# Kernel tuning notes

Measured on AMD Instinct MI355X. Metric: run time of the kernel, lower is better.

The kernel has to match this reference:

```python
import jax, jax.numpy as jnp
import numpy as np

N = 100000
E = 1600000
IN_DIM = 20
HID = 32
HEADS = 4
OUT = 64
NEG_SLOPE = 0.2


def _p(key, shape, scale=0.1):
    return jax.random.normal(key, shape, dtype=jnp.float32) * scale


def setup_inputs() -> dict:
    key = jax.random.key(0)
    ks = jax.random.split(key, 20)
    x = jax.random.normal(ks[0], (N, IN_DIM), dtype=jnp.float32)
    edge_index = jax.random.randint(ks[1], (2, E), 0, N, dtype=jnp.int32)
    edge_attr = jax.random.uniform(ks[2], (E, 1), dtype=jnp.float32)
    HC1 = HEADS * HID
    return {
        "x": x,
        "edge_index": edge_index,
        "edge_attr": edge_attr,
        "Wl1": _p(ks[3], (HC1, IN_DIM)), "bl1": jnp.zeros((HC1,), jnp.float32),
        "Wr1": _p(ks[4], (HC1, IN_DIM)), "br1": jnp.zeros((HC1,), jnp.float32),
        "We1": _p(ks[5], (HC1, 1)),
        "att1": _p(ks[6], (HEADS, HID)),
        "b1": jnp.zeros((HC1,), jnp.float32),
        "Wl2": _p(ks[7], (OUT, HC1)), "bl2": jnp.zeros((OUT,), jnp.float32),
        "Wr2": _p(ks[8], (OUT, HC1)), "br2": jnp.zeros((OUT,), jnp.float32),
        "We2": _p(ks[9], (OUT, 1)),
        "att2": _p(ks[10], (1, OUT)),
        "b2": jnp.zeros((OUT,), jnp.float32),
    }


def gatv2_conv(x, src, dst, edge_attr, Wl, bl, Wr, br, We, att, bias, heads, ch, concat):
    n = x.shape[0]
    # add self loops; edge_attr fill_value = mean (PyG default)
    loop = jnp.arange(n, dtype=src.dtype)
    src = jnp.concatenate([src, loop])
    dst = jnp.concatenate([dst, loop])
    ea_fill = jnp.broadcast_to(edge_attr.mean(axis=0, keepdims=True), (n, edge_attr.shape[1]))
    edge_attr = jnp.concatenate([edge_attr, ea_fill], axis=0)

    xl = (x @ Wl.T + bl).reshape(n, heads, ch)   # source transform [N,H,C]
    xr = (x @ Wr.T + br).reshape(n, heads, ch)   # target transform [N,H,C]
    ee = (edge_attr @ We.T).reshape(-1, heads, ch)  # edge embed [E',H,C]

    e = xl[src] + xr[dst] + ee                    # [E',H,C]
    e = jax.nn.leaky_relu(e, NEG_SLOPE)
    logits = jnp.einsum('ehc,hc->eh', e, att)     # [E',H]

    # segment softmax over destination nodes (every node has a self loop)
    mx = jax.ops.segment_max(logits, dst, num_segments=n)
    ex = jnp.exp(logits - mx[dst])
    denom = jax.ops.segment_sum(ex, dst, num_segments=n)
    alpha = ex / denom[dst]                       # [E',H]

    msg = xl[src] * alpha[:, :, None]             # [E',H,C]
    out = jax.ops.segment_sum(msg, dst, num_segments=n)  # [N,H,C]
    out = out.reshape(n, heads * ch) if concat else out.mean(axis=1)
    return out + bias


def reference(x, edge_index, edge_attr, Wl1, bl1, Wr1, br1, We1, att1, b1,
              Wl2, bl2, Wr2, br2, We2, att2, b2):
    src, dst = edge_index[0], edge_index[1]
    h = gatv2_conv(x, src, dst, edge_attr, Wl1, bl1, Wr1, br1, We1, att1, b1,
                   HEADS, HID, concat=True)
    h = jax.nn.elu(h)  # dropout is identity in eval mode
    out = gatv2_conv(h, src, dst, edge_attr, Wl2, bl2, Wr2, br2, We2, att2, b2,
                     1, OUT, concat=False)
    return out
```

## Files before the change

### kernel.cpp

```cpp
#include <hip/hip_runtime.h>
#include <cstdint>
#include <cstddef>

#define NNODES 100000
#define NEDGES 1600000
#define IN_DIM 20
#define HID    32
#define HEADS  4
#define HC1    128
#define OUTC   64
#define NEG    0.2f
#define NCHUNK ((NNODES + 255) / 256)
#define NBLK   ((NNODES + 63) / 64)

__device__ __forceinline__ float lrelu(float v) { return v >= 0.0f ? v : NEG * v; }

typedef _Float16 h2 __attribute__((ext_vector_type(2)));
union U4H { uint4 u; h2 h[4]; };
union U2H { uint2 u; h2 h[2]; };

__global__ void k_sum(const float* __restrict__ ea, int n, float* __restrict__ out) {
    float s = 0.0f;
    for (int i = blockIdx.x * blockDim.x + threadIdx.x; i < n; i += gridDim.x * blockDim.x)
        s += ea[i];
    #pragma unroll
    for (int off = 32; off > 0; off >>= 1) s += __shfl_down(s, off, 64);
    __shared__ float ls[4];
    int lane = threadIdx.x & 63, wid = threadIdx.x >> 6;
    if (lane == 0) ls[wid] = s;
    __syncthreads();
    if (threadIdx.x == 0) {
        float t = ls[0] + ls[1] + ls[2] + ls[3];
        atomicAdd(out, t);
    }
}

__global__ void k_hist(const int* __restrict__ ei, int* __restrict__ cnt) {
    int e = blockIdx.x * blockDim.x + threadIdx.x;
    if (e < NEDGES) atomicAdd(&cnt[ei[NEDGES + e]], 1);
}

__global__ void k_scan_chunk(const int* __restrict__ cnt, int* __restrict__ rowptr,
                             int* __restrict__ csums) {
    __shared__ int s[256];
    int i = blockIdx.x * 256 + threadIdx.x;
    int v = (i < NNODES) ? cnt[i] : 0;
    s[threadIdx.x] = v;
    __syncthreads();
    for (int off = 1; off < 256; off <<= 1) {
        int t = (threadIdx.x >= off) ? s[threadIdx.x - off] : 0;
        __syncthreads();
        s[threadIdx.x] += t;
        __syncthreads();
    }
    if (i < NNODES) rowptr[i] = s[threadIdx.x] - v;
    if (threadIdx.x == 255) csums[blockIdx.x] = s[255];
}

__global__ void k_scan_tops(int* __restrict__ csums) {
    __shared__ int s[512];
    int v = (threadIdx.x < NCHUNK) ? csums[threadIdx.x] : 0;
    s[threadIdx.x] = v;
    __syncthreads();
    for (int off = 1; off < 512; off <<= 1) {
        int t = (threadIdx.x >= off) ? s[threadIdx.x - off] : 0;
        __syncthreads();
        s[threadIdx.x] += t;
        __syncthreads();
    }
    if (threadIdx.x < NCHUNK) csums[threadIdx.x] = s[threadIdx.x] - v;
}

__global__ void k_scan_add(int* __restrict__ rowptr, const int* __restrict__ csums) {
    int i = blockIdx.x * 256 + threadIdx.x;
    if (i < NNODES) rowptr[i] += csums[blockIdx.x];
    if (i == 0) rowptr[NNODES] = NEDGES;
}

__global__ void k_scatter(const int* __restrict__ ei, const float* __restrict__ ea,
                          const int* __restrict__ rowptr, int* __restrict__ fill,
                          int2* __restrict__ cedge) {
    int e = blockIdx.x * blockDim.x + threadIdx.x;
    if (e >= NEDGES) return;
    int dst = ei[NEDGES + e];
    int pos = rowptr[dst] + atomicAdd(&fill[dst], 1);
    cedge[pos] = make_int2(ei[e], __float_as_int(ea[e]));
}

__global__ void k_prepB1(const float* __restrict__ Wl, const float* __restrict__ Wr,
                         float* __restrict__ Bt) {
    int idx = blockIdx.x * 256 + threadIdx.x;
    if (idx >= 20 * 256) return;
    int k = idx >> 8, c = idx & 255;
    Bt[idx] = (c < 128) ? Wl[c * IN_DIM + k] : Wr[(c - 128) * IN_DIM + k];
}
__global__ void k_prepB2(const float* __restrict__ Wl, const float* __restrict__ Wr,
                         float* __restrict__ Bt) {
    int idx = blockIdx.x * 256 + threadIdx.x;
    if (idx >= 128 * 128) return;
    int k = idx >> 7, c = idx & 127;
    Bt[idx] = (c < 64) ? Wl[c * HC1 + k] : Wr[(c - 64) * HC1 + k];
}

__global__ __launch_bounds__(256) void k_gemm1(
        const float* __restrict__ x, const float* __restrict__ Bt,
        const float* __restrict__ bl, const float* __restrict__ br,
        _Float16* __restrict__ xlh, _Float16* __restrict__ xrh) {
    __shared__ float sA[64 * IN_DIM];
    __shared__ float sB[IN_DIM * 256];
    int nb = blockIdx.x * 64;
    int tid = threadIdx.x;
    {
        size_t base = (size_t)nb * IN_DIM;
        size_t maxf = (size_t)NNODES * IN_DIM;
        for (int f = tid * 4; f < 64 * IN_DIM; f += 1024) {
            float4 v;
            if (base + f + 4 <= maxf) v = *(const float4*)(x + base + f);
            else                      v = *(const float4*)(x + maxf - 4);
            *(float4*)(sA + f) = v;
        }
    }
    for (int f = tid * 4; f < IN_DIM * 256; f += 1024)
        *(float4*)(sB + f) = *(const float4*)(Bt + f);
    __syncthreads();

    int tn = tid & 7, tc = tid >> 3;
    float acc[8][8];
    #pragma unroll
    for (int i = 0; i < 8; ++i)
        #pragma unroll
        for (int c = 0; c < 8; ++c) acc[i][c] = 0.0f;

    #pragma unroll
    for (int kt = 0; kt < 5; ++kt) {
        float4 a[8], b0[4], b1[4];
        #pragma unroll
        for (int i = 0; i < 8; ++i)
            a[i] = *(const float4*)(sA + (tn + 8 * i) * IN_DIM + kt * 4);
        #pragma unroll
        for (int j = 0; j < 4; ++j) {
            b0[j] = *(const float4*)(sB + (kt * 4 + j) * 256 + tc * 8);
            b1[j] = *(const float4*)(sB + (kt * 4 + j) * 256 + tc * 8 + 4);
        }
        #pragma unroll
        for (int i = 0; i < 8; ++i) {
            const float* ap = (const float*)&a[i];
            #pragma unroll
            for (int j = 0; j < 4; ++j) {
                float av = ap[j];
                const float* p0 = (const float*)&b0[j];
                const float* p1 = (const float*)&b1[j];
                #pragma unroll
                for (int c = 0; c < 4; ++c) {
                    acc[i][c]     += av * p0[c];
                    acc[i][c + 4] += av * p1[c];
                }
            }
        }
    }
    int c0 = tc * 8;
    float4 bias0, bias1;
    if (c0 < 128) {
        bias0 = *(const float4*)(bl + c0);
        bias1 = *(const float4*)(bl + c0 + 4);
    } else {
        bias0 = *(const float4*)(br + c0 - 128);
        bias1 = *(const float4*)(br + c0 - 124);
    }
    const float* q0 = (const float*)&bias0;
    const float* q1 = (const float*)&bias1;
    #pragma unroll
    for (int i = 0; i < 8; ++i) {
        int n = nb + tn + 8 * i;
        if (n >= NNODES) continue;
        float w[8];
        #pragma unroll
        for (int c = 0; c < 4; ++c) { w[c] = acc[i][c] + q0[c]; w[c + 4] = acc[i][c + 4] + q1[c]; }
        U4H ph;
        #pragma unroll
        for (int c = 0; c < 4; ++c) {
            h2 t; t.x = (_Float16)w[2 * c]; t.y = (_Float16)w[2 * c + 1];
            ph.h[c] = t;
        }
        if (c0 < 128) *(uint4*)(xlh + (size_t)n * HC1 + c0)       = ph.u;
        else          *(uint4*)(xrh + (size_t)n * HC1 + c0 - 128) = ph.u;
    }
}

__global__ __launch_bounds__(256) void k_gemm2(
        const float* __restrict__ h1, const float* __restrict__ Bt,
        const float* __restrict__ bl, const float* __restrict__ br,
        _Float16* __restrict__ xl2h, _Float16* __restrict__ xr2h) {
    __shared__ float sA[64 * 132];
    __shared__ float sB[32 * 128];
    int nb = blockIdx.x * 64;
    int tid = threadIdx.x;
    for (int f = tid * 4; f < 64 * HC1; f += 1024) {
        int node = f >> 7, k = f & 127;
        int gn = nb + node; if (gn >= NNODES) gn = NNODES - 1;
        float4 v = *(const float4*)(h1 + (size_t)gn * HC1 + k);
        *(float4*)(sA + node * 132 + k) = v;
    }
    int tn = tid & 7, tc = tid >> 3;
    float acc[8][4];
    #pragma unroll
    for (int i = 0; i < 8; ++i)
        #pragma unroll
        for (int c = 0; c < 4; ++c) acc[i][c] = 0.0f;

    for (int kc = 0; kc < 4; ++kc) {
        __syncthreads();
        for (int f = tid * 4; f < 32 * 128; f += 1024)
            *(float4*)(sB + f) = *(const float4*)(Bt + kc * 4096 + f);
        __syncthreads();
        #pragma unroll
        for (int ks = 0; ks < 8; ++ks) {
            int k0 = kc * 32 + ks * 4;
            float4 a[8], b[4];
            #pragma unroll
            for (int i = 0; i < 8; ++i)
                a[i] = *(const float4*)(sA + (tn + 8 * i) * 132 + k0);
            #pragma unroll
            for (int j = 0; j < 4; ++j)
                b[j] = *(const float4*)(sB + (ks * 4 + j) * 128 + tc * 4);
            #pragma unroll
            for (int i = 0; i < 8; ++i) {
                const float* ap = (const float*)&a[i];
                #pragma unroll
                for (int j = 0; j < 4; ++j) {
                    float av = ap[j];
                    const float* bp = (const float*)&b[j];
                    #pragma unroll
                    for (int c = 0; c < 4; ++c) acc[i][c] += av * bp[c];
                }
            }
        }
    }
    int c0 = tc * 4;
    float4 bias;
    if (c0 < 64) bias = *(const float4*)(bl + c0);
    else         bias = *(const float4*)(br + c0 - 64);
    const float* q = (const float*)&bias;
    #pragma unroll
    for (int i = 0; i < 8; ++i) {
        int n = nb + tn + 8 * i;
        if (n >= NNODES) continue;
        float w[4];
        #pragma unroll
        for (int c = 0; c < 4; ++c) w[c] = acc[i][c] + q[c];
        U2H ph;
        h2 t0; t0.x = (_Float16)w[0]; t0.y = (_Float16)w[1];
        h2 t1; t1.x = (_Float16)w[2]; t1.y = (_Float16)w[3];
        ph.h[0] = t0; ph.h[1] = t1;
        if (c0 < 64) *(uint2*)(xl2h + (size_t)n * OUTC + c0)      = ph.u;
        else         *(uint2*)(xr2h + (size_t)n * OUTC + c0 - 64) = ph.u;
    }
}

__global__ __launch_bounds__(256) void k_node1(
        const int* __restrict__ rowptr, const int2* __restrict__ cedge,
        const float* __restrict__ easum,
        const _Float16* __restrict__ xlh, const _Float16* __restrict__ xrh,
        const float* __restrict__ We, const float* __restrict__ att,
        const float* __restrict__ bias, float* __restrict__ h1) {
    int n = blockIdx.x * 4 + (threadIdx.x >> 6);
    if (n >= NNODES) return;
    int lane = threadIdx.x & 63;
    int g = lane >> 4;
    int q = lane & 15;
    int c = q * 8;
    U4H xru; xru.u = *(const uint4*)(xrh + (size_t)n * HC1 + c);
    float4 wf0 = *(const float4*)(We + c),  wf1 = *(const float4*)(We + c + 4);
    float4 af0 = *(const float4*)(att + c), af1 = *(const float4*)(att + c + 4);
    h2 we2[4], at2[4];
    we2[0].x = (_Float16)wf0.x; we2[0].y = (_Float16)wf0.y;
    we2[1].x = (_Float16)wf0.z; we2[1].y = (_Float16)wf0.w;
    we2[2].x = (_Float16)wf1.x; we2[2].y = (_Float16)wf1.y;
    we2[3].x = (_Float16)wf1.z; we2[3].y = (_Float16)wf1.w;
    at2[0].x = (_Float16)af0.x; at2[0].y = (_Float16)af0.y;
    at2[1].x = (_Float16)af0.z; at2[1].y = (_Float16)af0.w;
    at2[2].x = (_Float16)af1.x; at2[2].y = (_Float16)af1.y;
    at2[3].x = (_Float16)af1.z; at2[3].y = (_Float16)af1.w;
    h2 neg2; neg2.x = (_Float16)NEG; neg2.y = (_Float16)NEG;
    float s = 0.0f;
    float acc[8];
    #pragma unroll
    for (int k = 0; k < 8; ++k) acc[k] = 0.0f;
    int start = rowptr[n], end = rowptr[n + 1];
    int total = end - start + 1;
    float amean = easum[0] * (1.0f / (float)NEDGES);
    for (int base = 0; base < total; base += 4) {
        int o = base + g;
        int idx = start + o;
        int idxc = idx < NEDGES - 1 ? idx : NEDGES - 1;
        int2 ep = cedge[idxc];
        bool self  = (idx >= end);
        bool valid = (o < total);
        int src = self ? n : ep.x;
        float a = self ? amean : __int_as_float(ep.y);
        U4H xsu; xsu.u = *(const uint4*)(xlh + (size_t)src * HC1 + c);
        h2 a2; a2.x = (_Float16)a; a2.y = a2.x;
        h2 lacc;
        {
            h2 e = xsu.h[0] + a2 * we2[0] + xru.h[0];
            h2 l = __builtin_elementwise_max(e, neg2 * e);
            lacc = l * at2[0];
        }
        #pragma unroll
        for (int j = 1; j < 4; ++j) {
            h2 e = xsu.h[j] + a2 * we2[j] + xru.h[j];
            h2 l = __builtin_elementwise_max(e, neg2 * e);
            lacc += l * at2[j];
        }
        #pragma unroll
        for (int sh = 1; sh <= 2; sh <<= 1) {
            int lv = __builtin_bit_cast(int, lacc);
            int t = __shfl_xor(lv, sh, 64);
            lacc += __builtin_bit_cast(h2, t);
        }
        float p = (float)lacc.x + (float)lacc.y;
        float pe = valid ? __expf(p) : 0.0f;
        s += pe;
        acc[0] += pe * (float)xsu.h[0].x; acc[1] += pe * (float)xsu.h[0].y;
        acc[2] += pe * (float)xsu.h[1].x; acc[3] += pe * (float)xsu.h[1].y;
        acc[4] += pe * (float)xsu.h[2].x; acc[5] += pe * (float)xsu.h[2].y;
        acc[6] += pe * (float)xsu.h[3].x; acc[7] += pe * (float)xsu.h[3].y;
    }
    #pragma unroll
    for (int off = 16; off <= 32; off <<= 1) {
        s += __shfl_xor(s, off, 64);
        #pragma unroll
        for (int k = 0; k < 8; ++k) acc[k] += __shfl_xor(acc[k], off, 64);
    }
    if (g == 0) {
        float inv = 1.0f / s;
        float4 bi0 = *(const float4*)(bias + c), bi1 = *(const float4*)(bias + c + 4);
        const float* bq0 = (const float*)&bi0;
        const float* bq1 = (const float*)&bi1;
        float o[8];
        #pragma unroll
        for (int k = 0; k < 4; ++k) { o[k] = acc[k] * inv + bq0[k]; o[k + 4] = acc[k + 4] * inv + bq1[k]; }
        #pragma unroll
        for (int k = 0; k < 8; ++k) o[k] = o[k] > 0.0f ? o[k] : expm1f(o[k]);
        float4 o0 = make_float4(o[0], o[1], o[2], o[3]);
        float4 o1 = make_float4(o[4], o[5], o[6], o[7]);
        float4* op = (float4*)(h1 + (size_t)n * HC1 + c);
        op[0] = o0; op[1] = o1;
    }
}

__global__ __launch_bounds__(256) void k_node2(
        const int* __restrict__ rowptr, const int2* __restrict__ cedge,
        const float* __restrict__ easum,
        const _Float16* __restrict__ xl2h, const _Float16* __restrict__ xr2h,
        const float* __restrict__ We, const float* __restrict__ att,
        const float* __restrict__ bias, float* __restrict__ out) {
    int n = blockIdx.x * 4 + (threadIdx.x >> 6);
    if (n >= NNODES) return;
    int lane = threadIdx.x & 63;
    int g = lane >> 3;
    int q = lane & 7;
    int c = q * 8;
    U4H xru; xru.u = *(const uint4*)(xr2h + (size_t)n * OUTC + c);
    float4 wf0 = *(const float4*)(We + c),  wf1 = *(const float4*)(We + c + 4);
    float4 af0 = *(const float4*)(att + c), af1 = *(const float4*)(att + c + 4);
    h2 we2[4], at2[4];
    we2[0].x = (_Float16)wf0.x; we2[0].y = (_Float16)wf0.y;
    we2[1].x = (_Float16)wf0.z; we2[1].y = (_Float16)wf0.w;
    we2[2].x = (_Float16)wf1.x; we2[2].y = (_Float16)wf1.y;
    we2[3].x = (_Float16)wf1.z; we2[3].y = (_Float16)wf1.w;
    at2[0].x = (_Float16)af0.x; at2[0].y = (_Float16)af0.y;
    at2[1].x = (_Float16)af0.z; at2[1].y = (_Float16)af0.w;
    at2[2].x = (_Float16)af1.x; at2[2].y = (_Float16)af1.y;
    at2[3].x = (_Float16)af1.z; at2[3].y = (_Float16)af1.w;
    h2 neg2; neg2.x = (_Float16)NEG; neg2.y = (_Float16)NEG;
    float s = 0.0f;
    float acc[8];
    #pragma unroll
    for (int k = 0; k < 8; ++k) acc[k] = 0.0f;
    int start = rowptr[n], end = rowptr[n + 1];
    int total = end - start + 1;
    float amean = easum[0] * (1.0f / (float)NEDGES);
    for (int base = 0; base < total; base += 8) {
        int o = base + g;
        int idx = start + o;
        int idxc = idx < NEDGES - 1 ? idx : NEDGES - 1;
        int2 ep = cedge[idxc];
        bool self  = (idx >= end);
        bool valid = (o < total);
        int src = self ? n : ep.x;
        float a = self ? amean : __int_as_float(ep.y);
        U4H xsu; xsu.u = *(const uint4*)(xl2h + (size_t)src * OUTC + c);
        h2 a2; a2.x = (_Float16)a; a2.y = a2.x;
        h2 lacc;
        {
            h2 e = xsu.h[0] + a2 * we2[0] + xru.h[0];
            h2 l = __builtin_elementwise_max(e, neg2 * e);
            lacc = l * at2[0];
        }
        #pragma unroll
        for (int j = 1; j < 4; ++j) {
            h2 e = xsu.h[j] + a2 * we2[j] + xru.h[j];
            h2 l = __builtin_elementwise_max(e, neg2 * e);
            lacc += l * at2[j];
        }
        #pragma unroll
        for (int sh = 1; sh <= 4; sh <<= 1) {
            int lv = __builtin_bit_cast(int, lacc);
            int t = __shfl_xor(lv, sh, 64);
            lacc += __builtin_bit_cast(h2, t);
        }
        float p = (float)lacc.x + (float)lacc.y;
        float pe = valid ? __expf(p) : 0.0f;
        s += pe;
        acc[0] += pe * (float)xsu.h[0].x; acc[1] += pe * (float)xsu.h[0].y;
        acc[2] += pe * (float)xsu.h[1].x; acc[3] += pe * (float)xsu.h[1].y;
        acc[4] += pe * (float)xsu.h[2].x; acc[5] += pe * (float)xsu.h[2].y;
        acc[6] += pe * (float)xsu.h[3].x; acc[7] += pe * (float)xsu.h[3].y;
    }
    #pragma unroll
    for (int off = 8; off <= 32; off <<= 1) {
        s += __shfl_xor(s, off, 64);
        #pragma unroll
        for (int k = 0; k < 8; ++k) acc[k] += __shfl_xor(acc[k], off, 64);
    }
    if (g == 0) {
        float inv = 1.0f / s;
        float4 bi0 = *(const float4*)(bias + c), bi1 = *(const float4*)(bias + c + 4);
        const float* bq0 = (const float*)&bi0;
        const float* bq1 = (const float*)&bi1;
        float4 o0, o1;
        o0.x = acc[0] * inv + bq0[0];  o0.y = acc[1] * inv + bq0[1];
        o0.z = acc[2] * inv + bq0[2];  o0.w = acc[3] * inv + bq0[3];
        o1.x = acc[4] * inv + bq1[0];  o1.y = acc[5] * inv + bq1[1];
        o1.z = acc[6] * inv + bq1[2];  o1.w = acc[7] * inv + bq1[3];
        float4* op = (float4*)(out + (size_t)n * OUTC + c);
        op[0] = o0; op[1] = o1;
    }
}

extern "C" void kernel_launch(void* const* d_in, const int* in_sizes, int n_in,
                              void* d_out, int out_size, void* d_ws, size_t ws_size,
                              hipStream_t stream) {
    (void)in_sizes; (void)n_in; (void)out_size; (void)ws_size;
    const float* x    = (const float*)d_in[0];
    const int*   ei   = (const int*)d_in[1];
    const float* ea   = (const float*)d_in[2];
    const float* Wl1  = (const float*)d_in[3];
    const float* bl1  = (const float*)d_in[4];
    const float* Wr1  = (const float*)d_in[5];
    const float* br1  = (const float*)d_in[6];
    const float* We1  = (const float*)d_in[7];
    const float* att1 = (const float*)d_in[8];
    const float* b1   = (const float*)d_in[9];
    const float* Wl2  = (const float*)d_in[10];
    const float* bl2  = (const float*)d_in[11];
    const float* Wr2  = (const float*)d_in[12];
    const float* br2  = (const float*)d_in[13];
    const float* We2  = (const float*)d_in[14];
    const float* att2 = (const float*)d_in[15];
    const float* b2   = (const float*)d_in[16];
    float* out = (float*)d_out;

    char* wsb = (char*)d_ws;
    _Float16* xlh  = (_Float16*)wsb; wsb += (size_t)NNODES * HC1 * 2;
    _Float16* xrh  = (_Float16*)wsb; wsb += (size_t)NNODES * HC1 * 2;
    float*  h1     = (float*)wsb;    wsb += (size_t)NNODES * HC1 * 4;
    int2*   cedge  = (int2*)wsb;     wsb += (size_t)NEDGES * 8;
    int*    cnt    = (int*)wsb;      wsb += (size_t)NNODES * 4;
    int*    rowptr = (int*)wsb;      wsb += (size_t)(NNODES + 1) * 4;
    int*    fill   = (int*)wsb;      wsb += (size_t)NNODES * 4;
    int*    csums  = (int*)wsb;      wsb += 512 * 4;
    float*  easum  = (float*)wsb;    wsb += 16;
    float*  Bt1    = (float*)wsb;    wsb += 20 * 256 * 4;
    float*  Bt2    = (float*)wsb;    wsb += 128 * 128 * 4;
    _Float16* xl2h = xlh;
    _Float16* xr2h = xrh;

    hipMemsetAsync(easum, 0, sizeof(float), stream);
    hipMemsetAsync(cnt,  0, (size_t)NNODES * 4, stream);
    hipMemsetAsync(fill, 0, (size_t)NNODES * 4, stream);

    k_sum<<<256, 256, 0, stream>>>(ea, NEDGES, easum);
    k_hist<<<(NEDGES + 255) / 256, 256, 0, stream>>>(ei, cnt);
    k_prepB1<<<(20 * 256 + 255) / 256, 256, 0, stream>>>(Wl1, Wr1, Bt1);
    k_prepB2<<<(128 * 128 + 255) / 256, 256, 0, stream>>>(Wl2, Wr2, Bt2);
    k_scan_chunk<<<NCHUNK, 256, 0, stream>>>(cnt, rowptr, csums);
    k_scan_tops<<<1, 512, 0, stream>>>(csums);
    k_scan_add<<<NCHUNK, 256, 0, stream>>>(rowptr, csums);
    k_scatter<<<(NEDGES + 255) / 256, 256, 0, stream>>>(ei, ea, rowptr, fill, cedge);

    k_gemm1<<<NBLK, 256, 0, stream>>>(x, Bt1, bl1, br1, xlh, xrh);
    k_node1<<<(NNODES + 3) / 4, 256, 0, stream>>>(rowptr, cedge, easum,
                                                  xlh, xrh, We1, att1, b1, h1);

    k_gemm2<<<NBLK, 256, 0, stream>>>(h1, Bt2, bl2, br2, xl2h, xr2h);
    k_node2<<<(NNODES + 3) / 4, 256, 0, stream>>>(rowptr, cedge, easum,
                                                  xl2h, xr2h, We2, att2, b2, out);
}
```

Baseline: 545.9 us.

## Store layer-1 output in fp16, reuse histogram ranks, and unroll edge loops

Several independent changes. The hidden layer h1 is stored as fp16 instead of fp32, which halves its write and read traffic between k_node1 and k_gemm2. The histogram kernel records each edge's atomic rank, so the scatter no longer needs its own atomics or the fill buffer. The node kernels handle the self loop separately, outside the edge loop, and fold log2(e) into the attention weights so they can use exp2f. k_node1 also processes two edges per group per iteration to get more memory loads in flight. The cost is more fp16 rounding of the hidden activations, an extra 4-byte-per-edge rank buffer, and higher register pressure.

```diff
diff --git a/kernel.cpp b/kernel.cpp
--- a/kernel.cpp
+++ b/kernel.cpp
@@ -10,10 +10,9 @@
 #define HC1    128
 #define OUTC   64
 #define NEG    0.2f
+#define LOG2E  1.4426950408889634f
 #define NCHUNK ((NNODES + 255) / 256)
 #define NBLK   ((NNODES + 63) / 64)
-
-__device__ __forceinline__ float lrelu(float v) { return v >= 0.0f ? v : NEG * v; }
 
 typedef _Float16 h2 __attribute__((ext_vector_type(2)));
 union U4H { uint4 u; h2 h[4]; };
@@ -35,9 +34,10 @@
     }
 }
 
-__global__ void k_hist(const int* __restrict__ ei, int* __restrict__ cnt) {
+__global__ void k_hist(const int* __restrict__ ei, int* __restrict__ cnt,
+                       int* __restrict__ erank) {
     int e = blockIdx.x * blockDim.x + threadIdx.x;
-    if (e < NEDGES) atomicAdd(&cnt[ei[NEDGES + e]], 1);
+    if (e < NEDGES) erank[e] = atomicAdd(&cnt[ei[NEDGES + e]], 1);
 }
 
 __global__ void k_scan_chunk(const int* __restrict__ cnt, int* __restrict__ rowptr,
@@ -78,12 +78,12 @@
 }
 
 __global__ void k_scatter(const int* __restrict__ ei, const float* __restrict__ ea,
-                          const int* __restrict__ rowptr, int* __restrict__ fill,
+                          const int* __restrict__ rowptr, const int* __restrict__ erank,
                           int2* __restrict__ cedge) {
     int e = blockIdx.x * blockDim.x + threadIdx.x;
     if (e >= NEDGES) return;
     int dst = ei[NEDGES + e];
-    int pos = rowptr[dst] + atomicAdd(&fill[dst], 1);
+    int pos = rowptr[dst] + erank[e];
     cedge[pos] = make_int2(ei[e], __float_as_int(ea[e]));
 }
 
@@ -188,18 +188,24 @@
 }
 
 __global__ __launch_bounds__(256) void k_gemm2(
-        const float* __restrict__ h1, const float* __restrict__ Bt,
+        const _Float16* __restrict__ h1h, const float* __restrict__ Bt,
         const float* __restrict__ bl, const float* __restrict__ br,
         _Float16* __restrict__ xl2h, _Float16* __restrict__ xr2h) {
     __shared__ float sA[64 * 132];
     __shared__ float sB[32 * 128];
     int nb = blockIdx.x * 64;
     int tid = threadIdx.x;
-    for (int f = tid * 4; f < 64 * HC1; f += 1024) {
-        int node = f >> 7, k = f & 127;
+    for (int idx = tid * 8; idx < 64 * HC1; idx += 2048) {
+        int node = idx >> 7, k = idx & 127;
         int gn = nb + node; if (gn >= NNODES) gn = NNODES - 1;
-        float4 v = *(const float4*)(h1 + (size_t)gn * HC1 + k);
-        *(float4*)(sA + node * 132 + k) = v;
+        U4H v; v.u = *(const uint4*)(h1h + ((size_t)gn << 7) + k);
+        float4 f0, f1;
+        f0.x = (float)v.h[0].x; f0.y = (float)v.h[0].y;
+        f0.z = (float)v.h[1].x; f0.w = (float)v.h[1].y;
+        f1.x = (float)v.h[2].x; f1.y = (float)v.h[2].y;
+        f1.z = (float)v.h[3].x; f1.w = (float)v.h[3].y;
+        *(float4*)(sA + node * 132 + k)     = f0;
+        *(float4*)(sA + node * 132 + k + 4) = f1;
     }
     int tn = tid & 7, tc = tid >> 3;
     float acc[8][4];
@@ -262,14 +268,14 @@
         const float* __restrict__ easum,
         const _Float16* __restrict__ xlh, const _Float16* __restrict__ xrh,
         const float* __restrict__ We, const float* __restrict__ att,
-        const float* __restrict__ bias, float* __restrict__ h1) {
+        const float* __restrict__ bias, _Float16* __restrict__ h1h) {
     int n = blockIdx.x * 4 + (threadIdx.x >> 6);
     if (n >= NNODES) return;
     int lane = threadIdx.x & 63;
     int g = lane >> 4;
     int q = lane & 15;
     int c = q * 8;
-    U4H xru; xru.u = *(const uint4*)(xrh + (size_t)n * HC1 + c);
+    U4H xru; xru.u = *(const uint4*)(xrh + ((unsigned)n << 7) + c);
     float4 wf0 = *(const float4*)(We + c),  wf1 = *(const float4*)(We + c + 4);
     float4 af0 = *(const float4*)(att + c), af1 = *(const float4*)(att + c + 4);
     h2 we2[4], at2[4];
@@ -277,40 +283,31 @@
     we2[1].x = (_Float16)wf0.z; we2[1].y = (_Float16)wf0.w;
     we2[2].x = (_Float16)wf1.x; we2[2].y = (_Float16)wf1.y;
     we2[3].x = (_Float16)wf1.z; we2[3].y = (_Float16)wf1.w;
-    at2[0].x = (_Float16)af0.x; at2[0].y = (_Float16)af0.y;
-    at2[1].x = (_Float16)af0.z; at2[1].y = (_Float16)af0.w;
-    at2[2].x = (_Float16)af1.x; at2[2].y = (_Float16)af1.y;
-    at2[3].x = (_Float16)af1.z; at2[3].y = (_Float16)af1.w;
+    at2[0].x = (_Float16)(af0.x * LOG2E); at2[0].y = (_Float16)(af0.y * LOG2E);
+    at2[1].x = (_Float16)(af0.z * LOG2E); at2[1].y = (_Float16)(af0.w * LOG2E);
+    at2[2].x = (_Float16)(af1.x * LOG2E); at2[2].y = (_Float16)(af1.y * LOG2E);
+    at2[3].x = (_Float16)(af1.z * LOG2E); at2[3].y = (_Float16)(af1.w * LOG2E);
     h2 neg2; neg2.x = (_Float16)NEG; neg2.y = (_Float16)NEG;
     float s = 0.0f;
     float acc[8];
     #pragma unroll
     for (int k = 0; k < 8; ++k) acc[k] = 0.0f;
     int start = rowptr[n], end = rowptr[n + 1];
-    int total = end - start + 1;
-    float amean = easum[0] * (1.0f / (float)NEDGES);
-    for (int base = 0; base < total; base += 4) {
-        int o = base + g;
-        int idx = start + o;
-        int idxc = idx < NEDGES - 1 ? idx : NEDGES - 1;
-        int2 ep = cedge[idxc];
-        bool self  = (idx >= end);
-        bool valid = (o < total);
-        int src = self ? n : ep.x;
-        float a = self ? amean : __int_as_float(ep.y);
-        U4H xsu; xsu.u = *(const uint4*)(xlh + (size_t)src * HC1 + c);
-        h2 a2; a2.x = (_Float16)a; a2.y = a2.x;
+    int deg = end - start;
+
+    {
+        U4H xss; xss.u = *(const uint4*)(xlh + ((unsigned)n << 7) + c);
+        float amean = easum[0] * (1.0f / (float)NEDGES);
+        h2 a2; a2.x = (_Float16)amean; a2.y = a2.x;
         h2 lacc;
         {
-            h2 e = xsu.h[0] + a2 * we2[0] + xru.h[0];
-            h2 l = __builtin_elementwise_max(e, neg2 * e);
-            lacc = l * at2[0];
+            h2 e = xss.h[0] + a2 * we2[0] + xru.h[0];
+            lacc = __builtin_elementwise_max(e, neg2 * e) * at2[0];
         }
         #pragma unroll
         for (int j = 1; j < 4; ++j) {
-            h2 e = xsu.h[j] + a2 * we2[j] + xru.h[j];
-            h2 l = __builtin_elementwise_max(e, neg2 * e);
-            lacc += l * at2[j];
+            h2 e = xss.h[j] + a2 * we2[j] + xru.h[j];
+            lacc += __builtin_elementwise_max(e, neg2 * e) * at2[j];
         }
         #pragma unroll
         for (int sh = 1; sh <= 2; sh <<= 1) {
@@ -318,13 +315,77 @@
             int t = __shfl_xor(lv, sh, 64);
             lacc += __builtin_bit_cast(h2, t);
         }
-        float p = (float)lacc.x + (float)lacc.y;
-        float pe = valid ? __expf(p) : 0.0f;
-        s += pe;
-        acc[0] += pe * (float)xsu.h[0].x; acc[1] += pe * (float)xsu.h[0].y;
-        acc[2] += pe * (float)xsu.h[1].x; acc[3] += pe * (float)xsu.h[1].y;
-        acc[4] += pe * (float)xsu.h[2].x; acc[5] += pe * (float)xsu.h[2].y;
-        acc[6] += pe * (float)xsu.h[3].x; acc[7] += pe * (float)xsu.h[3].y;
+        if (g == 0) {
+            float pe = exp2f((float)lacc.x + (float)lacc.y);
+            s += pe;
+            acc[0] += pe * (float)xss.h[0].x; acc[1] += pe * (float)xss.h[0].y;
+            acc[2] += pe * (float)xss.h[1].x; acc[3] += pe * (float)xss.h[1].y;
+            acc[4] += pe * (float)xss.h[2].x; acc[5] += pe * (float)xss.h[2].y;
+            acc[6] += pe * (float)xss.h[3].x; acc[7] += pe * (float)xss.h[3].y;
+        }
+    }
+
+    for (int base = 0; base < deg; base += 8) {
+        int oA = base + g, oB = oA + 4;
+        int idxA = start + (oA < deg ? oA : deg - 1);
+        int idxB = start + (oB < deg ? oB : deg - 1);
+        int2 epA = cedge[idxA];
+        int2 epB = cedge[idxB];
+        bool vA = oA < deg, vB = oB < deg;
+        int srcA = vA ? epA.x : n;
+        int srcB = vB ? epB.x : n;
+        U4H xsA; xsA.u = *(const uint4*)(xlh + ((unsigned)srcA << 7) + c);
+        U4H xsB; xsB.u = *(const uint4*)(xlh + ((unsigned)srcB << 7) + c);
+        {
+            h2 a2; a2.x = (_Float16)__int_as_float(epA.y); a2.y = a2.x;
+            h2 lacc;
+            {
+                h2 e = xsA.h[0] + a2 * we2[0] + xru.h[0];
+                lacc = __builtin_elementwise_max(e, neg2 * e) * at2[0];
+            }
+            #pragma unroll
+            for (int j = 1; j < 4; ++j) {
+                h2 e = xsA.h[j] + a2 * we2[j] + xru.h[j];
+                lacc += __builtin_elementwise_max(e, neg2 * e) * at2[j];
+            }
+            #pragma unroll
+            for (int sh = 1; sh <= 2; sh <<= 1) {
+                int lv = __builtin_bit_cast(int, lacc);
+                int t = __shfl_xor(lv, sh, 64);
+                lacc += __builtin_bit_cast(h2, t);
+            }
+            float pe = vA ? exp2f((float)lacc.x + (float)lacc.y) : 0.0f;
+            s += pe;
+            acc[0] += pe * (float)xsA.h[0].x; acc[1] += pe * (float)xsA.h[0].y;
+            acc[2] += pe * (float)xsA.h[1].x; acc[3] += pe * (float)xsA.h[1].y;
+            acc[4] += pe * (float)xsA.h[2].x; acc[5] += pe * (float)xsA.h[2].y;
+            acc[6] += pe * (float)xsA.h[3].x; acc[7] += pe * (float)xsA.h[3].y;
+        }
+        {
+            h2 a2; a2.x = (_Float16)__int_as_float(epB.y); a2.y = a2.x;
+            h2 lacc;
+            {
+                h2 e = xsB.h[0] + a2 * we2[0] + xru.h[0];
+                lacc = __builtin_elementwise_max(e, neg2 * e) * at2[0];
+            }
+            #pragma unroll
+            for (int j = 1; j < 4; ++j) {
+                h2 e = xsB.h[j] + a2 * we2[j] + xru.h[j];
+                lacc += __builtin_elementwise_max(e, neg2 * e) * at2[j];
+            }
+            #pragma unroll
+            for (int sh = 1; sh <= 2; sh <<= 1) {
+                int lv = __builtin_bit_cast(int, lacc);
+                int t = __shfl_xor(lv, sh, 64);
+                lacc += __builtin_bit_cast(h2, t);
+            }
+            float pe = vB ? exp2f((float)lacc.x + (float)lacc.y) : 0.0f;
+            s += pe;
+            acc[0] += pe * (float)xsB.h[0].x; acc[1] += pe * (float)xsB.h[0].y;
+            acc[2] += pe * (float)xsB.h[1].x; acc[3] += pe * (float)xsB.h[1].y;
+            acc[4] += pe * (float)xsB.h[2].x; acc[5] += pe * (float)xsB.h[2].y;
+            acc[6] += pe * (float)xsB.h[3].x; acc[7] += pe * (float)xsB.h[3].y;
+        }
     }
     #pragma unroll
     for (int off = 16; off <= 32; off <<= 1) {
@@ -342,10 +403,13 @@
         for (int k = 0; k < 4; ++k) { o[k] = acc[k] * inv + bq0[k]; o[k + 4] = acc[k + 4] * inv + bq1[k]; }
         #pragma unroll
         for (int k = 0; k < 8; ++k) o[k] = o[k] > 0.0f ? o[k] : expm1f(o[k]);
-        float4 o0 = make_float4(o[0], o[1], o[2], o[3]);
-        float4 o1 = make_float4(o[4], o[5], o[6], o[7]);
-        float4* op = (float4*)(h1 + (size_t)n * HC1 + c);
-        op[0] = o0; op[1] = o1;
+        U4H ph;
+        #pragma unroll
+        for (int k = 0; k < 4; ++k) {
+            h2 t; t.x = (_Float16)o[2 * k]; t.y = (_Float16)o[2 * k + 1];
+            ph.h[k] = t;
+        }
+        *(uint4*)(h1h + ((unsigned)n << 7) + c) = ph.u;
     }
 }
 
@@ -361,7 +425,7 @@
     int g = lane >> 3;
     int q = lane & 7;
     int c = q * 8;
-    U4H xru; xru.u = *(const uint4*)(xr2h + (size_t)n * OUTC + c);
+    U4H xru; xru.u = *(const uint4*)(xr2h + ((unsigned)n << 6) + c);
     float4 wf0 = *(const float4*)(We + c),  wf1 = *(const float4*)(We + c + 4);
     float4 af0 = *(const float4*)(att + c), af1 = *(const float4*)(att + c + 4);
     h2 we2[4], at2[4];
@@ -369,40 +433,31 @@
     we2[1].x = (_Float16)wf0.z; we2[1].y = (_Float16)wf0.w;
     we2[2].x = (_Float16)wf1.x; we2[2].y = (_Float16)wf1.y;
     we2[3].x = (_Float16)wf1.z; we2[3].y = (_Float16)wf1.w;
-    at2[0].x = (_Float16)af0.x; at2[0].y = (_Float16)af0.y;
-    at2[1].x = (_Float16)af0.z; at2[1].y = (_Float16)af0.w;
-    at2[2].x = (_Float16)af1.x; at2[2].y = (_Float16)af1.y;
-    at2[3].x = (_Float16)af1.z; at2[3].y = (_Float16)af1.w;
+    at2[0].x = (_Float16)(af0.x * LOG2E); at2[0].y = (_Float16)(af0.y * LOG2E);
+    at2[1].x = (_Float16)(af0.z * LOG2E); at2[1].y = (_Float16)(af0.w * LOG2E);
+    at2[2].x = (_Float16)(af1.x * LOG2E); at2[2].y = (_Float16)(af1.y * LOG2E);
+    at2[3].x = (_Float16)(af1.z * LOG2E); at2[3].y = (_Float16)(af1.w * LOG2E);
     h2 neg2; neg2.x = (_Float16)NEG; neg2.y = (_Float16)NEG;
     float s = 0.0f;
     float acc[8];
     #pragma unroll
     for (int k = 0; k < 8; ++k) acc[k] = 0.0f;
     int start = rowptr[n], end = rowptr[n + 1];
-    int total = end - start + 1;
-    float amean = easum[0] * (1.0f / (float)NEDGES);
-    for (int base = 0; base < total; base += 8) {
-        int o = base + g;
-        int idx = start + o;
-        int idxc = idx < NEDGES - 1 ? idx : NEDGES - 1;
-        int2 ep = cedge[idxc];
-        bool self  = (idx >= end);
-        bool valid = (o < total);
-        int src = self ? n : ep.x;
-        float a = self ? amean : __int_as_float(ep.y);
-        U4H xsu; xsu.u = *(const uint4*)(xl2h + (size_t)src * OUTC + c);
-        h2 a2; a2.x = (_Float16)a; a2.y = a2.x;
+    int deg = end - start;
+
+    {
+        U4H xss; xss.u = *(const uint4*)(xl2h + ((unsigned)n << 6) + c);
+        float amean = easum[0] * (1.0f / (float)NEDGES);
+        h2 a2; a2.x = (_Float16)amean; a2.y = a2.x;
         h2 lacc;
         {
-            h2 e = xsu.h[0] + a2 * we2[0] + xru.h[0];
-            h2 l = __builtin_elementwise_max(e, neg2 * e);
-            lacc = l * at2[0];
+            h2 e = xss.h[0] + a2 * we2[0] + xru.h[0];
+            lacc = __builtin_elementwise_max(e, neg2 * e) * at2[0];
         }
         #pragma unroll
         for (int j = 1; j < 4; ++j) {
-            h2 e = xsu.h[j] + a2 * we2[j] + xru.h[j];
-            h2 l = __builtin_elementwise_max(e, neg2 * e);
-            lacc += l * at2[j];
+            h2 e = xss.h[j] + a2 * we2[j] + xru.h[j];
+            lacc += __builtin_elementwise_max(e, neg2 * e) * at2[j];
         }
         #pragma unroll
         for (int sh = 1; sh <= 4; sh <<= 1) {
@@ -410,8 +465,41 @@
             int t = __shfl_xor(lv, sh, 64);
             lacc += __builtin_bit_cast(h2, t);
         }
-        float p = (float)lacc.x + (float)lacc.y;
-        float pe = valid ? __expf(p) : 0.0f;
+        if (g == 0) {
+            float pe = exp2f((float)lacc.x + (float)lacc.y);
+            s += pe;
+            acc[0] += pe * (float)xss.h[0].x; acc[1] += pe * (float)xss.h[0].y;
+            acc[2] += pe * (float)xss.h[1].x; acc[3] += pe * (float)xss.h[1].y;
+            acc[4] += pe * (float)xss.h[2].x; acc[5] += pe * (float)xss.h[2].y;
+            acc[6] += pe * (float)xss.h[3].x; acc[7] += pe * (float)xss.h[3].y;
+        }
+    }
+
+    for (int base = 0; base < deg; base += 8) {
+        int o = base + g;
+        int idx = start + (o < deg ? o : deg - 1);
+        int2 ep = cedge[idx];
+        bool valid = o < deg;
+        int src = valid ? ep.x : n;
+        U4H xsu; xsu.u = *(const uint4*)(xl2h + ((unsigned)src << 6) + c);
+        h2 a2; a2.x = (_Float16)__int_as_float(ep.y); a2.y = a2.x;
+        h2 lacc;
+        {
+            h2 e = xsu.h[0] + a2 * we2[0] + xru.h[0];
+            lacc = __builtin_elementwise_max(e, neg2 * e) * at2[0];
+        }
+        #pragma unroll
+        for (int j = 1; j < 4; ++j) {
+            h2 e = xsu.h[j] + a2 * we2[j] + xru.h[j];
+            lacc += __builtin_elementwise_max(e, neg2 * e) * at2[j];
+        }
+        #pragma unroll
+        for (int sh = 1; sh <= 4; sh <<= 1) {
+            int lv = __builtin_bit_cast(int, lacc);
+            int t = __shfl_xor(lv, sh, 64);
+            lacc += __builtin_bit_cast(h2, t);
+        }
+        float pe = valid ? exp2f((float)lacc.x + (float)lacc.y) : 0.0f;
         s += pe;
         acc[0] += pe * (float)xsu.h[0].x; acc[1] += pe * (float)xsu.h[0].y;
         acc[2] += pe * (float)xsu.h[1].x; acc[3] += pe * (float)xsu.h[1].y;
@@ -465,11 +553,11 @@
     char* wsb = (char*)d_ws;
     _Float16* xlh  = (_Float16*)wsb; wsb += (size_t)NNODES * HC1 * 2;
     _Float16* xrh  = (_Float16*)wsb; wsb += (size_t)NNODES * HC1 * 2;
-    float*  h1     = (float*)wsb;    wsb += (size_t)NNODES * HC1 * 4;
+    _Float16* h1h  = (_Float16*)wsb; wsb += (size_t)NNODES * HC1 * 2;
     int2*   cedge  = (int2*)wsb;     wsb += (size_t)NEDGES * 8;
+    int*    erank  = (int*)wsb;      wsb += (size_t)NEDGES * 4;
     int*    cnt    = (int*)wsb;      wsb += (size_t)NNODES * 4;
     int*    rowptr = (int*)wsb;      wsb += (size_t)(NNODES + 1) * 4;
-    int*    fill   = (int*)wsb;      wsb += (size_t)NNODES * 4;
     int*    csums  = (int*)wsb;      wsb += 512 * 4;
     float*  easum  = (float*)wsb;    wsb += 16;
     float*  Bt1    = (float*)wsb;    wsb += 20 * 256 * 4;
@@ -478,23 +566,22 @@
     _Float16* xr2h = xrh;
 
     hipMemsetAsync(easum, 0, sizeof(float), stream);
-    hipMemsetAsync(cnt,  0, (size_t)NNODES * 4, stream);
-    hipMemsetAsync(fill, 0, (size_t)NNODES * 4, stream);
+    hipMemsetAsync(cnt, 0, (size_t)NNODES * 4, stream);
 
     k_sum<<<256, 256, 0, stream>>>(ea, NEDGES, easum);
-    k_hist<<<(NEDGES + 255) / 256, 256, 0, stream>>>(ei, cnt);
+    k_hist<<<(NEDGES + 255) / 256, 256, 0, stream>>>(ei, cnt, erank);
     k_prepB1<<<(20 * 256 + 255) / 256, 256, 0, stream>>>(Wl1, Wr1, Bt1);
     k_prepB2<<<(128 * 128 + 255) / 256, 256, 0, stream>>>(Wl2, Wr2, Bt2);
     k_scan_chunk<<<NCHUNK, 256, 0, stream>>>(cnt, rowptr, csums);
     k_scan_tops<<<1, 512, 0, stream>>>(csums);
     k_scan_add<<<NCHUNK, 256, 0, stream>>>(rowptr, csums);
-    k_scatter<<<(NEDGES + 255) / 256, 256, 0, stream>>>(ei, ea, rowptr, fill, cedge);
+    k_scatter<<<(NEDGES + 255) / 256, 256, 0, stream>>>(ei, ea, rowptr, erank, cedge);
 
     k_gemm1<<<NBLK, 256, 0, stream>>>(x, Bt1, bl1, br1, xlh, xrh);
     k_node1<<<(NNODES + 3) / 4, 256, 0, stream>>>(rowptr, cedge, easum,
-                                                  xlh, xrh, We1, att1, b1, h1);
-
-    k_gemm2<<<NBLK, 256, 0, stream>>>(h1, Bt2, bl2, br2, xl2h, xr2h);
+                                                  xlh, xrh, We1, att1, b1, h1h);
+
+    k_gemm2<<<NBLK, 256, 0, stream>>>(h1h, Bt2, bl2, br2, xl2h, xr2h);
     k_node2<<<(NNODES + 3) / 4, 256, 0, stream>>>(rowptr, cedge, easum,
                                                   xl2h, xr2h, We2, att2, b2, out);
 }
```

Result: faster. 476.1 us (-12.8%).
